# Optimization experiments

Measured on AMD Instinct MI355X. Metric: run time of the kernel, lower is better.

## Reference

```python
import jax, jax.numpy as jnp
import numpy as np

DIM = 1024
D_STATE = 16
EXPAND = 2
D_CONV = 4
D_INNER = DIM * EXPAND          # 2048
DT_RANK = (DIM + 15) // 16      # ceil(dim/16) = 64
BATCH = 2
SEQ = 1024


def setup_inputs() -> dict:
    key = jax.random.key(0)
    ks = jax.random.split(key, 8)
    s = 0.02
    A = jnp.broadcast_to(jnp.arange(1, D_STATE + 1, dtype=jnp.float32), (D_INNER, D_STATE))
    return {
        "x": jax.random.normal(ks[0], (BATCH, SEQ, DIM), jnp.float32),
        "in_w": jax.random.normal(ks[1], (2 * D_INNER, DIM), jnp.float32) * s,
        "conv_w": jax.random.normal(ks[2], (D_INNER, 1, D_CONV), jnp.float32) * s,   # depthwise conv kernel (OIH)
        "conv_b": jnp.zeros((D_INNER,), jnp.float32),
        "xproj_w": jax.random.normal(ks[3], (DT_RANK + 2 * D_STATE, D_INNER), jnp.float32) * s,
        "dt_w": jax.random.normal(ks[4], (D_INNER, DT_RANK), jnp.float32) * s,
        "dt_b": jax.random.normal(ks[5], (D_INNER,), jnp.float32) * s,
        "A_log": jnp.log(A),
        "D": jnp.ones((D_INNER,), jnp.float32),
        "out_w": jax.random.normal(ks[6], (DIM, D_INNER), jnp.float32) * s,
    }


def _selective_scan(u, delta, A, B, C, D):
    # u: (b, d_in, l); delta: (b, l, d_in); A: (d_in, n); B, C: (b, l, n); D: (d_in,)
    dA = jnp.exp(jnp.einsum('bld,dn->lbdn', delta, A))          # (l, b, d_in, n)
    dBu = jnp.einsum('bld,bln,bdl->lbdn', delta, B, u)          # (l, b, d_in, n)
    Ct = jnp.transpose(C, (1, 0, 2))                            # (l, b, n)

    def step(carry, inp):
        a, bu, c = inp
        carry = a * carry + bu                                  # (b, d_in, n)
        y = jnp.einsum('bdn,bn->bd', carry, c)
        return carry, y

    x0 = jnp.zeros(dA.shape[1:], dA.dtype)
    _, ys = jax.lax.scan(step, x0, (dA, dBu, Ct))               # ys: (l, b, d_in)
    y = jnp.transpose(ys, (1, 2, 0))                            # (b, d_in, l)
    return y + u * D[:, None]


def reference(x, in_w, conv_w, conv_b, xproj_w, dt_w, dt_b, A_log, D, out_w):
    b, l, d = x.shape
    xr = x @ in_w.T                                             # (b, l, 2*d_in)
    xx, res = jnp.split(xr, 2, axis=-1)
    xx = jnp.transpose(xx, (0, 2, 1))                           # (b, d_in, l)
    # causal depthwise conv: left-pad d_conv-1 == torch pad=d_conv-1 then [:, :, :l]
    xx = jax.lax.conv_general_dilated(
        xx, conv_w, window_strides=(1,), padding=[(D_CONV - 1, 0)],
        dimension_numbers=('NCH', 'OIH', 'NCH'), feature_group_count=D_INNER
    ) + conv_b[None, :, None]
    xx = jax.nn.silu(xx)
    A = -jnp.exp(A_log)
    x_dbl = jnp.einsum('bdl,kd->blk', xx, xproj_w)              # (b, l, dt_rank + 2n)
    delta, B, C = jnp.split(x_dbl, [DT_RANK, DT_RANK + D_STATE], axis=-1)
    delta = jax.nn.softplus(delta @ dt_w.T + dt_b)              # (b, l, d_in)
    y = _selective_scan(xx, delta, A, B, C, D)                  # (b, d_in, l)
    y = y * jax.nn.silu(jnp.transpose(res, (0, 2, 1)))
    return jnp.transpose(y, (0, 2, 1)) @ out_w.T                # (b, l, dim)
```

## Files before the change

kernel.cpp:

```cpp
#include <hip/hip_runtime.h>
#include <hip/hip_bf16.h>
#include <stdint.h>

#define DIM      1024
#define D_STATE  16
#define D_CONV   4
#define D_INNER  2048
#define DT_RANK  64
#define BATCH    2
#define SEQ      1024
#define MROWS    (BATCH * SEQ)
#define NPROJ    (2 * D_INNER)
#define XDBL_K   (DT_RANK + 2 * D_STATE)

#define LC       16
#define NC       (SEQ / LC)
#define SLANES   (BATCH * D_INNER * D_STATE)

typedef __attribute__((ext_vector_type(8))) short short8;
typedef __attribute__((ext_vector_type(4))) float f32x4;
typedef unsigned short ushort_t;

__device__ __forceinline__ unsigned short f2bf(float f) {
    __hip_bfloat16 b = __float2bfloat16(f);
    return *reinterpret_cast<unsigned short*>(&b);
}
__device__ __forceinline__ float bf2f(unsigned short u) {
    __hip_bfloat16 b;
    *reinterpret_cast<unsigned short*>(&b) = u;
    return __bfloat162float(b);
}

__device__ __forceinline__ void gload_lds16(const unsigned short* g, unsigned short* l) {
    __builtin_amdgcn_global_load_lds(
        (const __attribute__((address_space(1))) void*)g,
        (__attribute__((address_space(3))) void*)l,
        16, 0, 0);
}

#define SG0 524288
#define SG1 1048576
#define SG2 65536
#define SG3 32768
#define SG4 524288
#define SPLIT_GRANULES (SG0 + SG1 + SG2 + SG3 + SG4)

__global__ __launch_bounds__(256) void split_all(
    const float* __restrict__ x,   const float* __restrict__ in_w,
    const float* __restrict__ xpw, const float* __restrict__ dtw,
    const float* __restrict__ ow,
    ushort_t* __restrict__ xh,   ushort_t* __restrict__ xl,
    ushort_t* __restrict__ iwh,  ushort_t* __restrict__ iwl,
    ushort_t* __restrict__ xph,  ushort_t* __restrict__ xpl,
    ushort_t* __restrict__ dth,  ushort_t* __restrict__ dtl,
    ushort_t* __restrict__ owh,  ushort_t* __restrict__ owl)
{
    int g = blockIdx.x * 256 + threadIdx.x;
    const float* src; int K, rows_src; ushort_t *dh, *dl;
    if (g < SG0)                      { src = x;    K = 1024; rows_src = 2048; dh = xh;  dl = xl; }
    else if ((g -= SG0) < SG1)        { src = in_w; K = 1024; rows_src = 4096; dh = iwh; dl = iwl; }
    else if ((g -= SG1) < SG2)        { src = xpw;  K = 2048; rows_src = 96;   dh = xph; dl = xpl; }
    else if ((g -= SG2) < SG3)        { src = dtw;  K = 64;   rows_src = 2048; dh = dth; dl = dtl; }
    else                              { g -= SG3;   src = ow; K = 2048; rows_src = 1024; dh = owh; dl = owl; }

    const int kq = K >> 2;
    const int r = g / kq;
    const int k4 = (g - r * kq) << 2;
    float4 v = make_float4(0.f, 0.f, 0.f, 0.f);
    if (r < rows_src)
        v = *reinterpret_cast<const float4*>(src + (size_t)r * K + k4);
    const unsigned short h0 = f2bf(v.x), h1 = f2bf(v.y), h2 = f2bf(v.z), h3 = f2bf(v.w);
    const unsigned short l0 = f2bf(v.x - bf2f(h0)), l1 = f2bf(v.y - bf2f(h1));
    const unsigned short l2 = f2bf(v.z - bf2f(h2)), l3 = f2bf(v.w - bf2f(h3));
    *reinterpret_cast<ushort4*>(dh + (size_t)r * K + k4) = make_ushort4(h0, h1, h2, h3);
    *reinterpret_cast<ushort4*>(dl + (size_t)r * K + k4) = make_ushort4(l0, l1, l2, l3);
}

__device__ __forceinline__ short8 frag_ld(const unsigned short* base, int row, int slot) {
    const char* p = reinterpret_cast<const char*>(base) +
                    row * 128 + (((slot ^ (row & 7)) & 7) << 4);
    return *reinterpret_cast<const short8*>(p);
}

template <int EPI>
__global__ __launch_bounds__(256) void gemm_bf3(
    const ushort_t* __restrict__ Ahg, const ushort_t* __restrict__ Alg, int lda,
    const ushort_t* __restrict__ Bhg, const ushort_t* __restrict__ Blg, int ldb,
    float* __restrict__ C, int ldc, size_t czstride,
    const float* __restrict__ bias, int kLen)
{
    __shared__ unsigned short Ahs[128 * 64];
    __shared__ unsigned short Als[128 * 64];
    __shared__ unsigned short Bhs[128 * 64];
    __shared__ unsigned short Bls[128 * 64];

    const int tid = threadIdx.x;
    const int lane = tid & 63;
    const int w = tid >> 6;
    const int wr = w >> 1, wc = w & 1;
    const int fr = lane & 15, fg = lane >> 4;
    const int m0 = blockIdx.y * 128;
    const int n0 = blockIdx.x * 128;
    const int kOff = blockIdx.z * kLen;
    Ahg += kOff; Alg += kOff; Bhg += kOff; Blg += kOff;
    C += (size_t)blockIdx.z * czstride;

    f32x4 zero = {0.f, 0.f, 0.f, 0.f};
    f32x4 acc[4][4];
#pragma unroll
    for (int i = 0; i < 4; ++i)
#pragma unroll
        for (int j = 0; j < 4; ++j) acc[i][j] = zero;

    for (int k0 = 0; k0 < kLen; k0 += 64) {
#pragma unroll
        for (int it = 0; it < 4; ++it) {
            const int f = it * 256 + tid;
            const int row = f >> 3;
            const int gc = ((f & 7) ^ (row & 7)) << 3;
            const size_t ga = (size_t)(m0 + row) * lda + k0 + gc;
            const size_t gb = (size_t)(n0 + row) * ldb + k0 + gc;
            gload_lds16(Ahg + ga, &Ahs[f * 8]);
            gload_lds16(Alg + ga, &Als[f * 8]);
            gload_lds16(Bhg + gb, &Bhs[f * 8]);
            gload_lds16(Blg + gb, &Bls[f * 8]);
        }
        __syncthreads();

#pragma unroll
        for (int kk = 0; kk < 2; ++kk) {
            short8 ah[4], bh[4], xf[4];
#pragma unroll
            for (int i = 0; i < 4; ++i) {
                ah[i] = frag_ld(Ahs, wr * 64 + i * 16 + fr, kk * 4 + fg);
                bh[i] = frag_ld(Bhs, wc * 64 + i * 16 + fr, kk * 4 + fg);
            }
#pragma unroll
            for (int i = 0; i < 4; ++i)
#pragma unroll
                for (int j = 0; j < 4; ++j)
                    acc[i][j] = __builtin_amdgcn_mfma_f32_16x16x32_bf16(
                        ah[i], bh[j], acc[i][j], 0, 0, 0);
#pragma unroll
            for (int i = 0; i < 4; ++i)
                xf[i] = frag_ld(Bls, wc * 64 + i * 16 + fr, kk * 4 + fg);
#pragma unroll
            for (int i = 0; i < 4; ++i)
#pragma unroll
                for (int j = 0; j < 4; ++j)
                    acc[i][j] = __builtin_amdgcn_mfma_f32_16x16x32_bf16(
                        ah[i], xf[j], acc[i][j], 0, 0, 0);
#pragma unroll
            for (int i = 0; i < 4; ++i)
                xf[i] = frag_ld(Als, wr * 64 + i * 16 + fr, kk * 4 + fg);
#pragma unroll
            for (int i = 0; i < 4; ++i)
#pragma unroll
                for (int j = 0; j < 4; ++j)
                    acc[i][j] = __builtin_amdgcn_mfma_f32_16x16x32_bf16(
                        xf[i], bh[j], acc[i][j], 0, 0, 0);
        }
        __syncthreads();
    }

#pragma unroll
    for (int i = 0; i < 4; ++i) {
        const int mrow = m0 + wr * 64 + i * 16 + fg * 4;
#pragma unroll
        for (int j = 0; j < 4; ++j) {
            const int col = n0 + wc * 64 + j * 16 + fr;
#pragma unroll
            for (int r = 0; r < 4; ++r) {
                float v = acc[i][j][r];
                if constexpr (EPI == 1) {
                    v += bias[col];
                    v = (v > 20.f) ? v : log1pf(__expf(v));
                }
                C[(size_t)(mrow + r) * ldc + col] = v;
            }
        }
    }
}

__global__ __launch_bounds__(256) void conv_silu(
    const float* __restrict__ XR, const float* __restrict__ cw,
    const float* __restrict__ cb, ushort_t* __restrict__ Uh,
    ushort_t* __restrict__ Ul)
{
    const int idx = blockIdx.x * 256 + threadIdx.x;
    const int d = idx & (D_INNER - 1);
    const int m = idx >> 11;
    const int l = m & (SEQ - 1);

    float acc = cb[d];
#pragma unroll
    for (int j = 0; j < D_CONV; ++j) {
        const int ll = l - (D_CONV - 1) + j;
        if (ll >= 0)
            acc = fmaf(XR[(size_t)(m - (D_CONV - 1) + j) * NPROJ + d],
                       cw[d * D_CONV + j], acc);
    }
    const float s = acc / (1.f + __expf(-acc));
    const unsigned short h = f2bf(s);
    Uh[idx] = h;
    Ul[idx] = f2bf(s - bf2f(h));
}

__global__ __launch_bounds__(256) void scan_phase1(
    const float* __restrict__ DELTA, const ushort_t* __restrict__ Uh,
    const ushort_t* __restrict__ Ul, const float* __restrict__ XDBL,
    const float* __restrict__ A_log, float* __restrict__ P,
    float* __restrict__ HL)
{
    const int tid = threadIdx.x;
    const int d = blockIdx.x * 256 + tid;
    const int c = blockIdx.y;
    const int b = blockIdx.z;

    float a[16];
#pragma unroll
    for (int q = 0; q < 4; ++q) {
        const float4 v = *reinterpret_cast<const float4*>(A_log + (size_t)d * 16 + q * 4);
        a[q * 4 + 0] = -__expf(v.x);
        a[q * 4 + 1] = -__expf(v.y);
        a[q * 4 + 2] = -__expf(v.z);
        a[q * 4 + 3] = -__expf(v.w);
    }
    float h[16];
#pragma unroll
    for (int n = 0; n < 16; ++n) h[n] = 0.f;
    float sd = 0.f;
    const size_t base = (size_t)b * SEQ + (size_t)c * LC;

#pragma unroll 4
    for (int t = 0; t < LC; ++t) {
        const size_t m = base + t;
        const float delta = DELTA[m * D_INNER + d];
        const float u = bf2f(Uh[m * D_INNER + d]) + bf2f(Ul[m * D_INNER + d]);
        const float du = delta * u;
        const float* xb = XDBL + m * XDBL_K + DT_RANK;
        float bv[16];
#pragma unroll
        for (int n = 0; n < 16; ++n) bv[n] = xb[n];
        sd += delta;
#pragma unroll
        for (int n = 0; n < 16; ++n) {
            const float dA = __expf(delta * a[n]);
            h[n] = fmaf(dA, h[n], du * bv[n]);
        }
    }

    const size_t idx = (size_t)c * SLANES + ((size_t)b * D_INNER + d) * 16;
#pragma unroll
    for (int q = 0; q < 4; ++q) {
        float4 pv, hv;
        pv.x = __expf(a[q * 4 + 0] * sd);
        pv.y = __expf(a[q * 4 + 1] * sd);
        pv.z = __expf(a[q * 4 + 2] * sd);
        pv.w = __expf(a[q * 4 + 3] * sd);
        hv.x = h[q * 4 + 0]; hv.y = h[q * 4 + 1];
        hv.z = h[q * 4 + 2]; hv.w = h[q * 4 + 3];
        *reinterpret_cast<float4*>(&P[idx + q * 4]) = pv;
        *reinterpret_cast<float4*>(&HL[idx + q * 4]) = hv;
    }
}

__global__ __launch_bounds__(256) void scan_phase2(
    float* __restrict__ P, const float* __restrict__ HL)
{
    const int t = blockIdx.x * 256 + threadIdx.x;
    float h = 0.f;
#pragma unroll 4
    for (int c = 0; c < NC; ++c) {
        const size_t idx = (size_t)c * SLANES + t;
        const float p = P[idx];
        const float hl = HL[idx];
        P[idx] = h;
        h = fmaf(p, h, hl);
    }
}

__global__ __launch_bounds__(256) void scan_phase3(
    const float* __restrict__ DELTA, const ushort_t* __restrict__ Uh,
    const ushort_t* __restrict__ Ul, const float* __restrict__ XDBL,
    const float* __restrict__ XR, const float* __restrict__ A_log,
    const float* __restrict__ Dp, const float* __restrict__ H0,
    ushort_t* __restrict__ Yh, ushort_t* __restrict__ Yl)
{
    const int tid = threadIdx.x;
    const int d = blockIdx.x * 256 + tid;
    const int c = blockIdx.y;
    const int b = blockIdx.z;

    float a[16];
#pragma unroll
    for (int q = 0; q < 4; ++q) {
        const float4 v = *reinterpret_cast<const float4*>(A_log + (size_t)d * 16 + q * 4);
        a[q * 4 + 0] = -__expf(v.x);
        a[q * 4 + 1] = -__expf(v.y);
        a[q * 4 + 2] = -__expf(v.z);
        a[q * 4 + 3] = -__expf(v.w);
    }
    const float Dd = Dp[d];

    float h[16];
    const size_t idx0 = (size_t)c * SLANES + ((size_t)b * D_INNER + d) * 16;
#pragma unroll
    for (int q = 0; q < 4; ++q) {
        const float4 v = *reinterpret_cast<const float4*>(&H0[idx0 + q * 4]);
        h[q * 4 + 0] = v.x; h[q * 4 + 1] = v.y;
        h[q * 4 + 2] = v.z; h[q * 4 + 3] = v.w;
    }
    const size_t base = (size_t)b * SEQ + (size_t)c * LC;

#pragma unroll 4
    for (int t = 0; t < LC; ++t) {
        const size_t m = base + t;
        const float delta = DELTA[m * D_INNER + d];
        const float u = bf2f(Uh[m * D_INNER + d]) + bf2f(Ul[m * D_INNER + d]);
        const float du = delta * u;
        const float* xb = XDBL + m * XDBL_K + DT_RANK;
        float bv[16], cv[16];
#pragma unroll
        for (int n = 0; n < 16; ++n) bv[n] = xb[n];
#pragma unroll
        for (int n = 0; n < 16; ++n) cv[n] = xb[16 + n];

        float y0 = 0.f, y1 = 0.f, y2 = 0.f, y3 = 0.f;
#pragma unroll
        for (int n = 0; n < 4; ++n) {
            const float dA0 = __expf(delta * a[n]);
            const float dA1 = __expf(delta * a[n + 4]);
            const float dA2 = __expf(delta * a[n + 8]);
            const float dA3 = __expf(delta * a[n + 12]);
            h[n]      = fmaf(dA0, h[n],      du * bv[n]);
            h[n + 4]  = fmaf(dA1, h[n + 4],  du * bv[n + 4]);
            h[n + 8]  = fmaf(dA2, h[n + 8],  du * bv[n + 8]);
            h[n + 12] = fmaf(dA3, h[n + 12], du * bv[n + 12]);
            y0 = fmaf(h[n],      cv[n],      y0);
            y1 = fmaf(h[n + 4],  cv[n + 4],  y1);
            y2 = fmaf(h[n + 8],  cv[n + 8],  y2);
            y3 = fmaf(h[n + 12], cv[n + 12], y3);
        }
        const float y = (y0 + y1) + (y2 + y3) + u * Dd;
        const float r = XR[m * NPROJ + D_INNER + d];
        const float sr = r / (1.f + __expf(-r));
        const float yg = y * sr;
        const unsigned short hh = f2bf(yg);
        Yh[m * D_INNER + d] = hh;
        Yl[m * D_INNER + d] = f2bf(yg - bf2f(hh));
    }
}

__global__ __launch_bounds__(256) void reduce_xdbl(
    const float* __restrict__ PP, float* __restrict__ XDBL,
    ushort_t* __restrict__ XDh, ushort_t* __restrict__ XDl)
{
    const int t = blockIdx.x * 256 + threadIdx.x;
    const int m = t / XDBL_K;
    const int n = t - m * XDBL_K;
    float s = 0.f;
#pragma unroll
    for (int z = 0; z < 8; ++z)
        s += PP[(size_t)z * MROWS * 128 + (size_t)m * 128 + n];
    XDBL[t] = s;
    if (n < DT_RANK) {
        const unsigned short h = f2bf(s);
        XDh[(size_t)m * DT_RANK + n] = h;
        XDl[(size_t)m * DT_RANK + n] = f2bf(s - bf2f(h));
    }
}

__global__ __launch_bounds__(256) void reduce_out(
    const float* __restrict__ OP, float* __restrict__ out)
{
    const int t = blockIdx.x * 256 + threadIdx.x;
    const float4 a = *reinterpret_cast<const float4*>(OP + (size_t)t * 4);
    const float4 b = *reinterpret_cast<const float4*>(OP + (size_t)MROWS * DIM + (size_t)t * 4);
    float4 r;
    r.x = a.x + b.x; r.y = a.y + b.y; r.z = a.z + b.z; r.w = a.w + b.w;
    *reinterpret_cast<float4*>(out + (size_t)t * 4) = r;
}

extern "C" void kernel_launch(void* const* d_in, const int* in_sizes, int n_in,
                              void* d_out, int out_size, void* d_ws, size_t ws_size,
                              hipStream_t stream)
{
    const float* x       = (const float*)d_in[0];
    const float* in_w    = (const float*)d_in[1];
    const float* conv_w  = (const float*)d_in[2];
    const float* conv_b  = (const float*)d_in[3];
    const float* xproj_w = (const float*)d_in[4];
    const float* dt_w    = (const float*)d_in[5];
    const float* dt_b    = (const float*)d_in[6];
    const float* A_log   = (const float*)d_in[7];
    const float* Dp      = (const float*)d_in[8];
    const float* out_w   = (const float*)d_in[9];
    float* out = (float*)d_out;

    const size_t MF = 1024 * 1024;
    float* WF    = (float*)d_ws;
    float* XR    = WF;
    float* DELTA = WF + 8 * MF;
    float* XDBL  = WF + 12 * MF;
    float* P     = WF + 13 * MF;
    float* HL    = WF + 17 * MF;
    float* PP    = WF + 8 * MF;
    float* OP    = WF;

    ushort_t* UB  = (ushort_t*)(WF + 21 * MF);
    ushort_t* xh  = UB;
    ushort_t* xl  = UB + 2 * MF;
    ushort_t* iwh = UB + 4 * MF;
    ushort_t* iwl = UB + 8 * MF;
    ushort_t* Uh  = UB;
    ushort_t* Ul  = UB + 4 * MF;
    ushort_t* Yh  = UB + 8 * MF;
    ushort_t* Yl  = (ushort_t*)(WF + 17 * MF);
    ushort_t* xph = UB + 12 * MF;
    ushort_t* xpl = xph + 256 * 1024;
    ushort_t* dth = xpl + 256 * 1024;
    ushort_t* dtl = dth + 128 * 1024;
    ushort_t* owh = dtl + 128 * 1024;
    ushort_t* owl = owh + 2 * MF;
    ushort_t* XDh = owl + 2 * MF;
    ushort_t* XDl = XDh + 128 * 1024;

    const dim3 blk(256);

    split_all<<<SPLIT_GRANULES / 256, blk, 0, stream>>>(
        x, in_w, xproj_w, dt_w, out_w,
        xh, xl, iwh, iwl, xph, xpl, dth, dtl, owh, owl);

    gemm_bf3<0><<<dim3(NPROJ / 128, MROWS / 128, 1), blk, 0, stream>>>(
        xh, xl, DIM, iwh, iwl, DIM, XR, NPROJ, 0, nullptr, DIM);

    conv_silu<<<(MROWS * D_INNER) / 256, blk, 0, stream>>>(XR, conv_w, conv_b, Uh, Ul);

    gemm_bf3<0><<<dim3(1, MROWS / 128, 8), blk, 0, stream>>>(
        Uh, Ul, D_INNER, xph, xpl, D_INNER, PP, 128, (size_t)MROWS * 128, nullptr, D_INNER / 8);
    reduce_xdbl<<<(MROWS * XDBL_K) / 256, blk, 0, stream>>>(PP, XDBL, XDh, XDl);

    gemm_bf3<1><<<dim3(D_INNER / 128, MROWS / 128, 1), blk, 0, stream>>>(
        XDh, XDl, DT_RANK, dth, dtl, DT_RANK, DELTA, D_INNER, 0, dt_b, DT_RANK);

    scan_phase1<<<dim3(D_INNER / 256, NC, BATCH), blk, 0, stream>>>(
        DELTA, Uh, Ul, XDBL, A_log, P, HL);
    scan_phase2<<<SLANES / 256, blk, 0, stream>>>(P, HL);
    scan_phase3<<<dim3(D_INNER / 256, NC, BATCH), blk, 0, stream>>>(
        DELTA, Uh, Ul, XDBL, XR, A_log, Dp, P, Yh, Yl);

    gemm_bf3<0><<<dim3(DIM / 128, MROWS / 128, 2), blk, 0, stream>>>(
        Yh, Yl, D_INNER, owh, owl, D_INNER, OP, DIM, (size_t)MROWS * DIM, nullptr, D_INNER / 2);
    reduce_out<<<(MROWS * DIM / 4) / 256, blk, 0, stream>>>(OP, out);
}
```

Measured before the change: 228.3 us.

## Double-buffer GEMM K tiles at 32, deepen split-K, and lengthen scan chunks

The bf16x3 GEMM moves from a single-buffered 64-wide K tile to a double-buffered 32-wide K tile with a new swizzle. The next tile's global-to-LDS loads are issued before the MFMAs on the current tile, so memory latency can overlap with compute and one barrier per step is dropped. Split-K goes from 8 to 16 for the x_proj GEMM and from 2 to 4 for the output projection, with the reductions and workspace aliasing updated to match. The scan chunk length goes from 16 to 32, giving fewer chunks. The trade-off is more partial-sum traffic in the reductions, fewer MFMAs per barrier, and longer serial work per scan chunk.

```diff
diff --git a/kernel.cpp b/kernel.cpp
--- a/kernel.cpp
+++ b/kernel.cpp
@@ -13,7 +13,7 @@
 #define NPROJ    (2 * D_INNER)
 #define XDBL_K   (DT_RANK + 2 * D_STATE)
 
-#define LC       16
+#define LC       32
 #define NC       (SEQ / LC)
 #define SLANES   (BATCH * D_INNER * D_STATE)
 
@@ -76,9 +76,9 @@
     *reinterpret_cast<ushort4*>(dl + (size_t)r * K + k4) = make_ushort4(l0, l1, l2, l3);
 }
 
-__device__ __forceinline__ short8 frag_ld(const unsigned short* base, int row, int slot) {
+__device__ __forceinline__ short8 frag32(const ushort_t* base, int row, int slot) {
     const char* p = reinterpret_cast<const char*>(base) +
-                    row * 128 + (((slot ^ (row & 7)) & 7) << 4);
+                    row * 64 + (((slot ^ ((row >> 1) & 3)) & 3) << 4);
     return *reinterpret_cast<const short8*>(p);
 }
 
@@ -89,10 +89,10 @@
     float* __restrict__ C, int ldc, size_t czstride,
     const float* __restrict__ bias, int kLen)
 {
-    __shared__ unsigned short Ahs[128 * 64];
-    __shared__ unsigned short Als[128 * 64];
-    __shared__ unsigned short Bhs[128 * 64];
-    __shared__ unsigned short Bls[128 * 64];
+    __shared__ ushort_t Ahs[2][128 * 32];
+    __shared__ ushort_t Als[2][128 * 32];
+    __shared__ ushort_t Bhs[2][128 * 32];
+    __shared__ ushort_t Bls[2][128 * 32];
 
     const int tid = threadIdx.x;
     const int lane = tid & 63;
@@ -105,6 +105,17 @@
     Ahg += kOff; Alg += kOff; Bhg += kOff; Blg += kOff;
     C += (size_t)blockIdx.z * czstride;
 
+    const int g0 = tid, g1 = tid + 256;
+    const int r0 = g0 >> 2, s0 = g0 & 3;
+    const int r1 = g1 >> 2, s1 = g1 & 3;
+    const int c0 = (s0 ^ ((r0 >> 1) & 3)) << 3;
+    const int c1 = (s1 ^ ((r1 >> 1) & 3)) << 3;
+    const size_t a0 = (size_t)(m0 + r0) * lda + c0;
+    const size_t a1 = (size_t)(m0 + r1) * lda + c1;
+    const size_t b0 = (size_t)(n0 + r0) * ldb + c0;
+    const size_t b1 = (size_t)(n0 + r1) * ldb + c1;
+    const int l0 = g0 * 8, l1 = g1 * 8;
+
     f32x4 zero = {0.f, 0.f, 0.f, 0.f};
     f32x4 acc[4][4];
 #pragma unroll
@@ -112,54 +123,57 @@
 #pragma unroll
         for (int j = 0; j < 4; ++j) acc[i][j] = zero;
 
-    for (int k0 = 0; k0 < kLen; k0 += 64) {
-#pragma unroll
-        for (int it = 0; it < 4; ++it) {
-            const int f = it * 256 + tid;
-            const int row = f >> 3;
-            const int gc = ((f & 7) ^ (row & 7)) << 3;
-            const size_t ga = (size_t)(m0 + row) * lda + k0 + gc;
-            const size_t gb = (size_t)(n0 + row) * ldb + k0 + gc;
-            gload_lds16(Ahg + ga, &Ahs[f * 8]);
-            gload_lds16(Alg + ga, &Als[f * 8]);
-            gload_lds16(Bhg + gb, &Bhs[f * 8]);
-            gload_lds16(Blg + gb, &Bls[f * 8]);
+    auto STAGE = [&](int buf, int kt) {
+        const int k0 = kt * 32;
+        gload_lds16(Ahg + a0 + k0, &Ahs[buf][l0]);
+        gload_lds16(Ahg + a1 + k0, &Ahs[buf][l1]);
+        gload_lds16(Alg + a0 + k0, &Als[buf][l0]);
+        gload_lds16(Alg + a1 + k0, &Als[buf][l1]);
+        gload_lds16(Bhg + b0 + k0, &Bhs[buf][l0]);
+        gload_lds16(Bhg + b1 + k0, &Bhs[buf][l1]);
+        gload_lds16(Blg + b0 + k0, &Bls[buf][l0]);
+        gload_lds16(Blg + b1 + k0, &Bls[buf][l1]);
+    };
+
+    const int nt = kLen >> 5;
+    STAGE(0, 0);
+    __syncthreads();
+
+    for (int t = 0; t < nt; ++t) {
+        const int cur = t & 1;
+        if (t + 1 < nt) STAGE(cur ^ 1, t + 1);
+
+        short8 ah[4], bh[4], xf[4];
+#pragma unroll
+        for (int i = 0; i < 4; ++i) {
+            ah[i] = frag32(Ahs[cur], wr * 64 + i * 16 + fr, fg);
+            bh[i] = frag32(Bhs[cur], wc * 64 + i * 16 + fr, fg);
         }
-        __syncthreads();
-
-#pragma unroll
-        for (int kk = 0; kk < 2; ++kk) {
-            short8 ah[4], bh[4], xf[4];
-#pragma unroll
-            for (int i = 0; i < 4; ++i) {
-                ah[i] = frag_ld(Ahs, wr * 64 + i * 16 + fr, kk * 4 + fg);
-                bh[i] = frag_ld(Bhs, wc * 64 + i * 16 + fr, kk * 4 + fg);
-            }
-#pragma unroll
-            for (int i = 0; i < 4; ++i)
-#pragma unroll
-                for (int j = 0; j < 4; ++j)
-                    acc[i][j] = __builtin_amdgcn_mfma_f32_16x16x32_bf16(
-                        ah[i], bh[j], acc[i][j], 0, 0, 0);
-#pragma unroll
-            for (int i = 0; i < 4; ++i)
-                xf[i] = frag_ld(Bls, wc * 64 + i * 16 + fr, kk * 4 + fg);
-#pragma unroll
-            for (int i = 0; i < 4; ++i)
-#pragma unroll
-                for (int j = 0; j < 4; ++j)
-                    acc[i][j] = __builtin_amdgcn_mfma_f32_16x16x32_bf16(
-                        ah[i], xf[j], acc[i][j], 0, 0, 0);
-#pragma unroll
-            for (int i = 0; i < 4; ++i)
-                xf[i] = frag_ld(Als, wr * 64 + i * 16 + fr, kk * 4 + fg);
-#pragma unroll
-            for (int i = 0; i < 4; ++i)
-#pragma unroll
-                for (int j = 0; j < 4; ++j)
-                    acc[i][j] = __builtin_amdgcn_mfma_f32_16x16x32_bf16(
-                        xf[i], bh[j], acc[i][j], 0, 0, 0);
-        }
+#pragma unroll
+        for (int i = 0; i < 4; ++i)
+#pragma unroll
+            for (int j = 0; j < 4; ++j)
+                acc[i][j] = __builtin_amdgcn_mfma_f32_16x16x32_bf16(
+                    ah[i], bh[j], acc[i][j], 0, 0, 0);
+#pragma unroll
+        for (int i = 0; i < 4; ++i)
+            xf[i] = frag32(Bls[cur], wc * 64 + i * 16 + fr, fg);
+#pragma unroll
+        for (int i = 0; i < 4; ++i)
+#pragma unroll
+            for (int j = 0; j < 4; ++j)
+                acc[i][j] = __builtin_amdgcn_mfma_f32_16x16x32_bf16(
+                    ah[i], xf[j], acc[i][j], 0, 0, 0);
+#pragma unroll
+        for (int i = 0; i < 4; ++i)
+            xf[i] = frag32(Als[cur], wr * 64 + i * 16 + fr, fg);
+#pragma unroll
+        for (int i = 0; i < 4; ++i)
+#pragma unroll
+            for (int j = 0; j < 4; ++j)
+                acc[i][j] = __builtin_amdgcn_mfma_f32_16x16x32_bf16(
+                    xf[i], bh[j], acc[i][j], 0, 0, 0);
+
         __syncthreads();
     }
 
@@ -361,7 +375,7 @@
     const int n = t - m * XDBL_K;
     float s = 0.f;
 #pragma unroll
-    for (int z = 0; z < 8; ++z)
+    for (int z = 0; z < 16; ++z)
         s += PP[(size_t)z * MROWS * 128 + (size_t)m * 128 + n];
     XDBL[t] = s;
     if (n < DT_RANK) {
@@ -375,11 +389,14 @@
     const float* __restrict__ OP, float* __restrict__ out)
 {
     const int t = blockIdx.x * 256 + threadIdx.x;
-    const float4 a = *reinterpret_cast<const float4*>(OP + (size_t)t * 4);
-    const float4 b = *reinterpret_cast<const float4*>(OP + (size_t)MROWS * DIM + (size_t)t * 4);
-    float4 r;
-    r.x = a.x + b.x; r.y = a.y + b.y; r.z = a.z + b.z; r.w = a.w + b.w;
-    *reinterpret_cast<float4*>(out + (size_t)t * 4) = r;
+    float4 s = *reinterpret_cast<const float4*>(OP + (size_t)t * 4);
+#pragma unroll
+    for (int z = 1; z < 4; ++z) {
+        const float4 v = *reinterpret_cast<const float4*>(
+            OP + (size_t)z * MROWS * DIM + (size_t)t * 4);
+        s.x += v.x; s.y += v.y; s.z += v.z; s.w += v.w;
+    }
+    *reinterpret_cast<float4*>(out + (size_t)t * 4) = s;
 }
 
 extern "C" void kernel_launch(void* const* d_in, const int* in_sizes, int n_in,
@@ -403,9 +420,9 @@
     float* XR    = WF;
     float* DELTA = WF + 8 * MF;
     float* XDBL  = WF + 12 * MF;
+    float* PP    = WF + 13 * MF;
     float* P     = WF + 13 * MF;
     float* HL    = WF + 17 * MF;
-    float* PP    = WF + 8 * MF;
     float* OP    = WF;
 
     ushort_t* UB  = (ushort_t*)(WF + 21 * MF);
@@ -437,8 +454,8 @@
 
     conv_silu<<<(MROWS * D_INNER) / 256, blk, 0, stream>>>(XR, conv_w, conv_b, Uh, Ul);
 
-    gemm_bf3<0><<<dim3(1, MROWS / 128, 8), blk, 0, stream>>>(
-        Uh, Ul, D_INNER, xph, xpl, D_INNER, PP, 128, (size_t)MROWS * 128, nullptr, D_INNER / 8);
+    gemm_bf3<0><<<dim3(1, MROWS / 128, 16), blk, 0, stream>>>(
+        Uh, Ul, D_INNER, xph, xpl, D_INNER, PP, 128, (size_t)MROWS * 128, nullptr, D_INNER / 16);
     reduce_xdbl<<<(MROWS * XDBL_K) / 256, blk, 0, stream>>>(PP, XDBL, XDh, XDl);
 
     gemm_bf3<1><<<dim3(D_INNER / 128, MROWS / 128, 1), blk, 0, stream>>>(
@@ -450,7 +467,7 @@
     scan_phase3<<<dim3(D_INNER / 256, NC, BATCH), blk, 0, stream>>>(
         DELTA, Uh, Ul, XDBL, XR, A_log, Dp, P, Yh, Yl);
 
-    gemm_bf3<0><<<dim3(DIM / 128, MROWS / 128, 2), blk, 0, stream>>>(
-        Yh, Yl, D_INNER, owh, owl, D_INNER, OP, DIM, (size_t)MROWS * DIM, nullptr, D_INNER / 2);
+    gemm_bf3<0><<<dim3(DIM / 128, MROWS / 128, 4), blk, 0, stream>>>(
+        Yh, Yl, D_INNER, owh, owl, D_INNER, OP, DIM, (size_t)MROWS * DIM, nullptr, D_INNER / 4);
     reduce_out<<<(MROWS * DIM / 4) / 256, blk, 0, stream>>>(OP, out);
 }
```

After: 234.0 us. +2.5%, slower.
